# Optimization experiments

Hardware: AMD Instinct MI355X
Metric: run time of the kernel (lower is better)

Reference implementation:

```python
import jax, jax.numpy as jnp
import numpy as np

D_MODEL = 2048
NUM_HEADS = 16
D_KV = D_MODEL // NUM_HEADS
THETA = 10000.0


def apply_rope(x, pos):
    # x: [B, H, S, d_kv], pos: [S] int
    d = x.shape[-1]
    inv_freq = 1.0 / (THETA ** (jnp.arange(0, d, 2, dtype=jnp.float32) / d))  # [d/2]
    ang = pos.astype(jnp.float32)[:, None] * inv_freq[None, :]  # [S, d/2]
    cos, sin = jnp.cos(ang), jnp.sin(ang)  # broadcast over B,H
    x1 = x[..., 0::2]
    x2 = x[..., 1::2]
    r1 = x1 * cos - x2 * sin
    r2 = x1 * sin + x2 * cos
    return jnp.stack([r1, r2], axis=-1).reshape(x.shape)


def setup_inputs() -> dict:
    key = jax.random.key(0)
    k = jax.random.split(key, 5)
    B, S = 2, 2048
    x = jax.random.normal(k[0], (B, S, D_MODEL), dtype=jnp.float32)
    scale = 1.0 / np.sqrt(D_MODEL)
    Wq = jax.random.normal(k[1], (D_MODEL, D_MODEL), dtype=jnp.float32) * scale
    Wk = jax.random.normal(k[2], (D_MODEL, D_MODEL), dtype=jnp.float32) * scale
    Wv = jax.random.normal(k[3], (D_MODEL, D_MODEL), dtype=jnp.float32) * scale
    Wo = jax.random.normal(k[4], (D_MODEL, D_MODEL), dtype=jnp.float32) * scale
    token_position = jnp.arange(S, dtype=jnp.int64 if jax.config.jax_enable_x64 else jnp.int32)
    return {"x": x, "Wq": Wq, "Wk": Wk, "Wv": Wv, "Wo": Wo, "token_position": token_position}


def reference(x, Wq, Wk, Wv, Wo, token_position):
    B, S, _ = x.shape
    def heads(y):
        return y.reshape(B, S, NUM_HEADS, D_KV).transpose(0, 2, 1, 3)  # [B,H,S,d]
    Q = heads(jnp.einsum('bsd,df->bsf', x, Wq))
    K = heads(jnp.einsum('bsd,df->bsf', x, Wk))
    V = heads(jnp.einsum('bsd,df->bsf', x, Wv))
    Q = apply_rope(Q, token_position)
    K = apply_rope(K, token_position)
    scale = 1.0 / jnp.sqrt(jnp.asarray(D_KV, dtype=x.dtype))
    scores = jnp.einsum('bhqd,bhkd->bhqk', Q, K) * scale  # [B,H,S,S]
    causal = jnp.tril(jnp.ones((S, S), dtype=bool))
    scores = jnp.where(causal, scores, -jnp.inf)
    attn = jax.nn.softmax(scores, axis=-1)
    out = jnp.einsum('bhqk,bhkd->bhqd', attn, V)  # [B,H,S,d]
    out = out.transpose(0, 2, 1, 3).reshape(B, S, D_MODEL)
    return jnp.einsum('bsd,df->bsf', out, Wo)
```

## Files before the change

kernel.cpp:

```cpp
#include <hip/hip_runtime.h>
#include <hip/hip_bf16.h>

#define S 2048
#define DM 2048
#define NH 16
#define DH 128

typedef __attribute__((ext_vector_type(8))) short short8;
typedef __attribute__((ext_vector_type(4))) float floatx4;
typedef unsigned short u16;
typedef unsigned int u32;

__device__ __forceinline__ u16 f2bf(float f) {
  union { float f; u32 u; } v; v.f = f;
  u32 r = v.u + 0x7fffu + ((v.u >> 16) & 1u);
  return (u16)(r >> 16);
}
__device__ __forceinline__ u32 pack2(float lo, float hi) {
  float2 f; f.x = lo; f.y = hi;
  __hip_bfloat162 h = __float22bfloat162_rn(f);
  union { __hip_bfloat162 h; u32 u; } c; c.h = h;
  return c.u;
}

__device__ __forceinline__ floatx4 mfma16(short8 a, short8 b, floatx4 c) {
  return __builtin_amdgcn_mfma_f32_16x16x32_bf16(a, b, c, 0, 0, 0);
}

__device__ __forceinline__ void async_cp16(const u16* g, u16* l) {
  __builtin_amdgcn_global_load_lds(
      (const __attribute__((address_space(1))) void*)g,
      (__attribute__((address_space(3))) void*)l, 16, 0, 0);
}

__global__ void conv_x_k(const float* __restrict__ x, u16* __restrict__ xb) {
  int gid = blockIdx.x * 256 + threadIdx.x;
  float4 v = ((const float4*)x)[gid];
  uint2 p; p.x = pack2(v.x, v.y); p.y = pack2(v.z, v.w);
  ((uint2*)xb)[gid] = p;
}

__global__ void conv_w_k(const float* __restrict__ W0, const float* __restrict__ W1,
                         const float* __restrict__ W2, const float* __restrict__ W3,
                         u16* __restrict__ out) {
  __shared__ float tile[32][33];
  const float* W = blockIdx.z == 0 ? W0 : blockIdx.z == 1 ? W1 : blockIdx.z == 2 ? W2 : W3;
  u16* O = out + (size_t)blockIdx.z * DM * DM;
  int tx = threadIdx.x & 31, ty = threadIdx.x >> 5;
  int k0 = blockIdx.y * 32, n0 = blockIdx.x * 32;
#pragma unroll
  for (int j = 0; j < 4; j++)
    tile[ty + j * 8][tx] = W[(size_t)(k0 + ty + j * 8) * DM + n0 + tx];
  __syncthreads();
#pragma unroll
  for (int j = 0; j < 4; j++)
    O[(size_t)(n0 + ty + j * 8) * DM + k0 + tx] = f2bf(tile[tx][ty + j * 8]);
}

#define BM 256
#define BN 256
#define BK 64

#define BARRIER __builtin_amdgcn_s_barrier()
#define SB __builtin_amdgcn_sched_barrier(0)
#define LGKM0 asm volatile("s_waitcnt lgkmcnt(0)" ::: "memory")

#define STG_A(q, j, koff) \
  async_cp16(pAg + (size_t)(j) * 64 * DM + (koff), &As[q][soff + (j) * 4096])
#define STG_B(q, j, koff) \
  async_cp16(pBg + (size_t)(j) * 64 * DM + (koff), &Bs[q][soff + (j) * 4096])

#define PH0(p, q, koff, PRE) { \
    a0k0 = *(const short8*)&As[p][awb + xk0]; \
    a0k1 = *(const short8*)&As[p][awb + xk1]; \
    a1k0 = *(const short8*)&As[p][awb + 1024 + xk0]; \
    a1k1 = *(const short8*)&As[p][awb + 1024 + xk1]; \
    a2k0 = *(const short8*)&As[p][awb + 2048 + xk0]; \
    a2k1 = *(const short8*)&As[p][awb + 2048 + xk1]; \
    a3k0 = *(const short8*)&As[p][awb + 3072 + xk0]; \
    a3k1 = *(const short8*)&As[p][awb + 3072 + xk1]; \
    b0k0 = *(const short8*)&Bs[p][bwb + xk0]; \
    b0k1 = *(const short8*)&Bs[p][bwb + xk1]; \
    b1k0 = *(const short8*)&Bs[p][bwb + 1024 + xk0]; \
    b1k1 = *(const short8*)&Bs[p][bwb + 1024 + xk1]; \
    if (PRE) { STG_A(q, 0, koff); STG_A(q, 1, koff); \
               STG_A(q, 2, koff); STG_A(q, 3, koff); } \
    BARRIER; LGKM0; SB; \
    __builtin_amdgcn_s_setprio(1); \
    acc[0][0] = mfma16(a0k0, b0k0, acc[0][0]); \
    acc[1][0] = mfma16(a1k0, b0k0, acc[1][0]); \
    acc[2][0] = mfma16(a2k0, b0k0, acc[2][0]); \
    acc[3][0] = mfma16(a3k0, b0k0, acc[3][0]); \
    acc[0][1] = mfma16(a0k0, b1k0, acc[0][1]); \
    acc[1][1] = mfma16(a1k0, b1k0, acc[1][1]); \
    acc[2][1] = mfma16(a2k0, b1k0, acc[2][1]); \
    acc[3][1] = mfma16(a3k0, b1k0, acc[3][1]); \
    acc[0][0] = mfma16(a0k1, b0k1, acc[0][0]); \
    acc[1][0] = mfma16(a1k1, b0k1, acc[1][0]); \
    acc[2][0] = mfma16(a2k1, b0k1, acc[2][0]); \
    acc[3][0] = mfma16(a3k1, b0k1, acc[3][0]); \
    acc[0][1] = mfma16(a0k1, b1k1, acc[0][1]); \
    acc[1][1] = mfma16(a1k1, b1k1, acc[1][1]); \
    acc[2][1] = mfma16(a2k1, b1k1, acc[2][1]); \
    acc[3][1] = mfma16(a3k1, b1k1, acc[3][1]); \
    __builtin_amdgcn_s_setprio(0); \
    BARRIER; }

#define PH1(p, q, koff, PRE) { \
    b2k0 = *(const short8*)&Bs[p][bwb + 2048 + xk0]; \
    b2k1 = *(const short8*)&Bs[p][bwb + 2048 + xk1]; \
    b3k0 = *(const short8*)&Bs[p][bwb + 3072 + xk0]; \
    b3k1 = *(const short8*)&Bs[p][bwb + 3072 + xk1]; \
    if (PRE) { STG_B(q, 0, koff); STG_B(q, 1, koff); \
               STG_B(q, 2, koff); STG_B(q, 3, koff); } \
    BARRIER; LGKM0; SB; \
    __builtin_amdgcn_s_setprio(1); \
    acc[0][2] = mfma16(a0k0, b2k0, acc[0][2]); \
    acc[1][2] = mfma16(a1k0, b2k0, acc[1][2]); \
    acc[2][2] = mfma16(a2k0, b2k0, acc[2][2]); \
    acc[3][2] = mfma16(a3k0, b2k0, acc[3][2]); \
    acc[0][3] = mfma16(a0k0, b3k0, acc[0][3]); \
    acc[1][3] = mfma16(a1k0, b3k0, acc[1][3]); \
    acc[2][3] = mfma16(a2k0, b3k0, acc[2][3]); \
    acc[3][3] = mfma16(a3k0, b3k0, acc[3][3]); \
    acc[0][2] = mfma16(a0k1, b2k1, acc[0][2]); \
    acc[1][2] = mfma16(a1k1, b2k1, acc[1][2]); \
    acc[2][2] = mfma16(a2k1, b2k1, acc[2][2]); \
    acc[3][2] = mfma16(a3k1, b2k1, acc[3][2]); \
    acc[0][3] = mfma16(a0k1, b3k1, acc[0][3]); \
    acc[1][3] = mfma16(a1k1, b3k1, acc[1][3]); \
    acc[2][3] = mfma16(a2k1, b3k1, acc[2][3]); \
    acc[3][3] = mfma16(a3k1, b3k1, acc[3][3]); \
    __builtin_amdgcn_s_setprio(0); \
    BARRIER; }

#define PH2(p) { \
    a0k0 = *(const short8*)&As[p][awb + 4096 + xk0]; \
    a0k1 = *(const short8*)&As[p][awb + 4096 + xk1]; \
    a1k0 = *(const short8*)&As[p][awb + 5120 + xk0]; \
    a1k1 = *(const short8*)&As[p][awb + 5120 + xk1]; \
    a2k0 = *(const short8*)&As[p][awb + 6144 + xk0]; \
    a2k1 = *(const short8*)&As[p][awb + 6144 + xk1]; \
    a3k0 = *(const short8*)&As[p][awb + 7168 + xk0]; \
    a3k1 = *(const short8*)&As[p][awb + 7168 + xk1]; \
    BARRIER; LGKM0; SB; \
    __builtin_amdgcn_s_setprio(1); \
    acc[4][0] = mfma16(a0k0, b0k0, acc[4][0]); \
    acc[5][0] = mfma16(a1k0, b0k0, acc[5][0]); \
    acc[6][0] = mfma16(a2k0, b0k0, acc[6][0]); \
    acc[7][0] = mfma16(a3k0, b0k0, acc[7][0]); \
    acc[4][1] = mfma16(a0k0, b1k0, acc[4][1]); \
    acc[5][1] = mfma16(a1k0, b1k0, acc[5][1]); \
    acc[6][1] = mfma16(a2k0, b1k0, acc[6][1]); \
    acc[7][1] = mfma16(a3k0, b1k0, acc[7][1]); \
    acc[4][0] = mfma16(a0k1, b0k1, acc[4][0]); \
    acc[5][0] = mfma16(a1k1, b0k1, acc[5][0]); \
    acc[6][0] = mfma16(a2k1, b0k1, acc[6][0]); \
    acc[7][0] = mfma16(a3k1, b0k1, acc[7][0]); \
    acc[4][1] = mfma16(a0k1, b1k1, acc[4][1]); \
    acc[5][1] = mfma16(a1k1, b1k1, acc[5][1]); \
    acc[6][1] = mfma16(a2k1, b1k1, acc[6][1]); \
    acc[7][1] = mfma16(a3k1, b1k1, acc[7][1]); \
    __builtin_amdgcn_s_setprio(0); \
    BARRIER; }

#define PH3(PRE) { \
    __builtin_amdgcn_s_setprio(1); \
    acc[4][2] = mfma16(a0k0, b2k0, acc[4][2]); \
    acc[5][2] = mfma16(a1k0, b2k0, acc[5][2]); \
    acc[6][2] = mfma16(a2k0, b2k0, acc[6][2]); \
    acc[7][2] = mfma16(a3k0, b2k0, acc[7][2]); \
    acc[4][3] = mfma16(a0k0, b3k0, acc[4][3]); \
    acc[5][3] = mfma16(a1k0, b3k0, acc[5][3]); \
    acc[6][3] = mfma16(a2k0, b3k0, acc[6][3]); \
    acc[7][3] = mfma16(a3k0, b3k0, acc[7][3]); \
    acc[4][2] = mfma16(a0k1, b2k1, acc[4][2]); \
    acc[5][2] = mfma16(a1k1, b2k1, acc[5][2]); \
    acc[6][2] = mfma16(a2k1, b2k1, acc[6][2]); \
    acc[7][2] = mfma16(a3k1, b2k1, acc[7][2]); \
    acc[4][3] = mfma16(a0k1, b3k1, acc[4][3]); \
    acc[5][3] = mfma16(a1k1, b3k1, acc[5][3]); \
    acc[6][3] = mfma16(a2k1, b3k1, acc[6][3]); \
    acc[7][3] = mfma16(a3k1, b3k1, acc[7][3]); \
    __builtin_amdgcn_s_setprio(0); SB; \
    if (PRE) { asm volatile("s_waitcnt vmcnt(0)" ::: "memory"); BARRIER; SB; } }

#define TILE(p, q, koff, PRE) \
    PH0(p, q, koff, PRE) PH1(p, q, koff, PRE) PH2(p) PH3(PRE)

__global__ __launch_bounds__(512, 2)
void gemm_k(const u16* __restrict__ A, const u16* __restrict__ Wt,
            u16* __restrict__ oQ, u16* __restrict__ oK, u16* __restrict__ oV,
            const int* __restrict__ tp)
{
  __shared__ u16 As[2][BM * BK];
  __shared__ u16 Bs[2][BN * BK];
  const int t = threadIdx.x;
  const int w = t >> 6, lane = t & 63;
  const int l16 = lane & 15, quad = lane >> 4;
  const int wr = w >> 2, wc = w & 3;
  const int m0 = blockIdx.y * BM, n0 = blockIdx.x * BN;
  const u16* Bt = Wt + (size_t)blockIdx.z * DM * DM;

  const int srow = t >> 3;
  const int sc = ((t & 7) ^ (srow & 7)) * 8;
  const u16* pAg = A + (size_t)(m0 + srow) * DM + sc;
  const u16* pBg = Bt + (size_t)(n0 + srow) * DM + sc;
  const int soff = t * 8;

  const int awb = (wr * 128 + l16) * 64;
  const int bwb = (wc * 64 + l16) * 64;
  const int xk0 = ((quad) ^ (l16 & 7)) << 3;
  const int xk1 = ((4 + quad) ^ (l16 & 7)) << 3;

  floatx4 acc[8][4] = {};
  short8 a0k0, a0k1, a1k0, a1k1, a2k0, a2k1, a3k0, a3k1;
  short8 b0k0, b0k1, b1k0, b1k1, b2k0, b2k1, b3k0, b3k1;

#pragma unroll
  for (int j = 0; j < 4; j++) STG_A(0, j, 0);
#pragma unroll
  for (int j = 0; j < 4; j++) STG_B(0, j, 0);
  SB;
  asm volatile("s_waitcnt vmcnt(0)" ::: "memory");
  BARRIER; SB;

  for (int it = 0; it < 16; ++it) {
    const int kA = (2 * it + 1) * 64;
    const int kB = (2 * it + 2) * 64;
    TILE(0, 1, kA, 1)
    TILE(1, 0, kB, it < 15)
  }

  const int mwb = m0 + wr * 128;
  const int nwb = n0 + wc * 64;
  if ((int)blockIdx.z == 2) {
#pragma unroll
    for (int mi = 0; mi < 8; mi++) {
      int m = mwb + mi * 16 + quad * 4;
      int b = m >> 11, s = m & (S - 1);
#pragma unroll
      for (int ni = 0; ni < 4; ni++) {
        int f = nwb + ni * 16 + l16;
        int h = f >> 7, dh = f & (DH - 1);
        uint2 pk; pk.x = pack2(acc[mi][ni][0], acc[mi][ni][1]);
        pk.y = pack2(acc[mi][ni][2], acc[mi][ni][3]);
        *(uint2*)&oV[((size_t)(b * NH + h) * DH + dh) * S + s] = pk;
      }
    }
  } else {
    u16* Out = ((int)blockIdx.z == 0) ? oQ : oK;
    const float qs = ((int)blockIdx.z == 0) ? 0.12752780f : 1.0f;
#pragma unroll
    for (int mi = 0; mi < 8; mi++) {
#pragma unroll
      for (int r = 0; r < 4; r++) {
        int m = mwb + mi * 16 + quad * 4 + r;
        int b = m >> 11, s = m & (S - 1);
        int ps = tp[s];
#pragma unroll
        for (int ni = 0; ni < 4; ni++) {
          int f = nwb + ni * 16 + l16;
          int h = f >> 7, dh = f & (DH - 1);
          float own = acc[mi][ni][r];
          float oth = __shfl_xor(own, 1, 64);
          float fr = __expf((float)(dh & ~1) * (-9.210340371976184f / 128.0f));
          float ang = (float)ps * fr;
          float sn, cs; __sincosf(ang, &sn, &cs);
          float res = (dh & 1) ? (oth * sn + own * cs) : (own * cs - oth * sn);
          Out[((size_t)(b * NH + h) * S + s) * DH + dh] = f2bf(res * qs);
        }
      }
    }
  }
}

__global__ __launch_bounds__(256, 4)
void oproj_k(const u16* __restrict__ A, const u16* __restrict__ Wt,
             float* __restrict__ oO)
{
  __shared__ u16 As2[128 * 32];
  __shared__ u16 Bs2[128 * 32];
  const int t = threadIdx.x;
  const int w = t >> 6, lane = t & 63;
  const int l16 = lane & 15, quad = lane >> 4;
  const int m0 = blockIdx.y * 128, n0 = blockIdx.x * 128;
  const int wm = (w >> 1) * 64, wn = (w & 1) * 64;
  const u16* Bt = Wt + (size_t)3 * DM * DM;

  const u16* pA[2]; const u16* pB[2]; u16* lA[2]; u16* lB[2];
#pragma unroll
  for (int i = 0; i < 2; i++) {
    int unit = i * 256 + t;
    int row = unit >> 2, s = unit & 3;
    int c = s ^ ((row >> 1) & 3);
    pA[i] = A + (size_t)(m0 + row) * DM + c * 8;
    pB[i] = Bt + (size_t)(n0 + row) * DM + c * 8;
    lA[i] = &As2[unit * 8];
    lB[i] = &Bs2[unit * 8];
  }

  floatx4 acc[4][4] = {};

  for (int k0 = 0; k0 < DM; k0 += 32) {
#pragma unroll
    for (int i = 0; i < 2; i++) {
      async_cp16(pA[i] + k0, lA[i]);
      async_cp16(pB[i] + k0, lB[i]);
    }
    __syncthreads();
    short8 af[4], bfr[4];
#pragma unroll
    for (int i = 0; i < 4; i++) {
      int row = wm + i * 16 + l16;
      af[i] = *(short8*)&As2[(row * 4 + (quad ^ ((row >> 1) & 3))) * 8];
    }
#pragma unroll
    for (int i = 0; i < 4; i++) {
      int row = wn + i * 16 + l16;
      bfr[i] = *(short8*)&Bs2[(row * 4 + (quad ^ ((row >> 1) & 3))) * 8];
    }
#pragma unroll
    for (int mi = 0; mi < 4; mi++)
#pragma unroll
      for (int ni = 0; ni < 4; ni++)
        acc[mi][ni] = mfma16(af[mi], bfr[ni], acc[mi][ni]);
    __syncthreads();
  }

#pragma unroll
  for (int mi = 0; mi < 4; mi++) {
    int m = m0 + wm + mi * 16 + quad * 4;
#pragma unroll
    for (int ni = 0; ni < 4; ni++) {
      int n = n0 + wn + ni * 16 + l16;
#pragma unroll
      for (int r = 0; r < 4; r++)
        oO[(size_t)(m + r) * DM + n] = acc[mi][ni][r];
    }
  }
}

__global__ __launch_bounds__(256, 4)
void attn_k(const u16* __restrict__ Q, const u16* __restrict__ K,
            const u16* __restrict__ Vt, u16* __restrict__ O)
{
  __shared__ u16 Ks[64 * 128];
  __shared__ u16 Vs[128 * 64];
  __shared__ u16 P[4][16 * 64];
  const int t = threadIdx.x, w = t >> 6, lane = t & 63;
  const int l16 = lane & 15, quad = lane >> 4;
  const int task = blockIdx.x;
  const int bh = task & 31, b = bh >> 4, h = bh & 15;
  const int g = 31 - (task >> 5);
  const int qg = g * 64;
  const int qt = qg + w * 16;
  const u16* Qb = Q + (size_t)bh * S * DH;
  const u16* Kb = K + (size_t)bh * S * DH;
  const u16* Vb = Vt + (size_t)bh * DH * S;
  u16* Pw = P[w];
  const int pxor = l16 & 7;

  const u16* pK[4]; u16* lK[4];
  const u16* pV[4]; u16* lV[4];
#pragma unroll
  for (int j = 0; j < 4; j++) {
    int kr = w * 16 + j * 4 + (lane >> 4);
    int ks = lane & 15;
    int kc = ks ^ (kr & 15);
    pK[j] = Kb + (size_t)kr * DH + kc * 8;
    lK[j] = &Ks[kr * 128 + ks * 8];
    int vr = w * 32 + j * 8 + (lane >> 3);
    int vs = lane & 7;
    int vc = vs ^ (vr & 7);
    pV[j] = Vb + (size_t)vr * S + vc * 8;
    lV[j] = &Vs[vr * 64 + vs * 8];
  }

  short8 aq[4];
#pragma unroll
  for (int kc = 0; kc < 4; kc++)
    aq[kc] = *(const short8*)&Qb[(size_t)(qt + l16) * DH + kc * 32 + quad * 8];

  floatx4 o[8] = {};
  float lsum = 0.0f;
  const int kend = qg + 64;

  for (int k0 = 0; k0 < kend; k0 += 64) {
#pragma unroll
    for (int j = 0; j < 4; j++) async_cp16(pK[j] + (size_t)k0 * DH, lK[j]);
#pragma unroll
    for (int j = 0; j < 4; j++) async_cp16(pV[j] + k0, lV[j]);
    __syncthreads();

    floatx4 sc[4] = {};
    __builtin_amdgcn_s_setprio(1);
#pragma unroll
    for (int hh = 0; hh < 4; hh++) {
      int row = hh * 16 + l16;
#pragma unroll
      for (int kc = 0; kc < 4; kc++) {
        short8 kf = *(short8*)&Ks[row * 128 + (((kc * 4 + quad) ^ l16) << 3)];
        sc[hh] = mfma16(kf, aq[kc], sc[hh]);
      }
    }
    __builtin_amdgcn_s_setprio(0);
    if (k0 + 64 > qt) {
#pragma unroll
      for (int hh = 0; hh < 4; hh++)
#pragma unroll
        for (int r = 0; r < 4; r++) {
          int j = k0 + hh * 16 + quad * 4 + r;
          if (j > qt + l16) sc[hh][r] = -3.0e38f;
        }
    }
#pragma unroll
    for (int hh = 0; hh < 4; hh++) {
      float e0 = __builtin_amdgcn_exp2f(fminf(sc[hh][0], 44.0f));
      float e1 = __builtin_amdgcn_exp2f(fminf(sc[hh][1], 44.0f));
      float e2 = __builtin_amdgcn_exp2f(fminf(sc[hh][2], 44.0f));
      float e3 = __builtin_amdgcn_exp2f(fminf(sc[hh][3], 44.0f));
      lsum += (e0 + e1) + (e2 + e3);
      uint2 pk; pk.x = pack2(e0, e1); pk.y = pack2(e2, e3);
      int su = (2 * hh + (quad >> 1)) ^ pxor;
      *(uint2*)&Pw[l16 * 64 + su * 8 + (quad & 1) * 4] = pk;
    }
    asm volatile("s_waitcnt lgkmcnt(0)" ::: "memory");
    __builtin_amdgcn_s_setprio(1);
#pragma unroll
    for (int c = 0; c < 2; c++) {
      short8 pf = *(short8*)&Pw[l16 * 64 + (((4 * c + quad) ^ pxor) << 3)];
#pragma unroll
      for (int t8 = 0; t8 < 8; t8++) {
        int row = t8 * 16 + l16;
        short8 av = *(short8*)&Vs[row * 64 + (((c * 4 + quad) ^ (l16 & 7)) << 3)];
        o[t8] = mfma16(av, pf, o[t8]);
      }
    }
    __builtin_amdgcn_s_setprio(0);
    __syncthreads();
  }

  float l = lsum + __shfl_xor(lsum, 16, 64);
  l += __shfl_xor(l, 32, 64);
  float inv = __builtin_amdgcn_rcpf(l);
#pragma unroll
  for (int t8 = 0; t8 < 8; t8++) {
    uint2 pa;
    pa.x = pack2(o[t8][0] * inv, o[t8][1] * inv);
    pa.y = pack2(o[t8][2] * inv, o[t8][3] * inv);
    *(uint2*)&O[((size_t)(b * S + qt + l16)) * DM + h * DH + t8 * 16 + quad * 4] = pa;
  }
}

extern "C" void kernel_launch(void* const* d_in, const int* in_sizes, int n_in,
                              void* d_out, int out_size, void* d_ws, size_t ws_size,
                              hipStream_t stream) {
  const float* x  = (const float*)d_in[0];
  const float* Wq = (const float*)d_in[1];
  const float* Wk = (const float*)d_in[2];
  const float* Wv = (const float*)d_in[3];
  const float* Wo = (const float*)d_in[4];
  const int*   tp = (const int*)d_in[5];

  char* ws = (char*)d_ws;
  u16* Wt = (u16*)ws;
  u16* xb = (u16*)(ws + 33554432);
  u16* Qb = (u16*)(ws + 50331648);
  u16* Kb = (u16*)(ws + 67108864);
  u16* Vb = (u16*)(ws + 83886080);
  u16* Ob = (u16*)(ws + 100663296);

  conv_x_k<<<8192, 256, 0, stream>>>(x, xb);
  conv_w_k<<<dim3(64, 64, 4), 256, 0, stream>>>(Wq, Wk, Wv, Wo, Wt);
  gemm_k<<<dim3(8, 16, 3), 512, 0, stream>>>(xb, Wt, Qb, Kb, Vb, tp);
  attn_k<<<1024, 256, 0, stream>>>(Qb, Kb, Vb, Ob);
  oproj_k<<<dim3(16, 32), 256, 0, stream>>>(Ob, Wt, (float*)d_out);
}
```

Baseline: 378.3 us.

## Deepen GEMM prefetch: load tile k+2 into same buffer after reads finish

Restructures the double-buffered QKV projection GEMM so both buffers are filled up front, and each tile's next-next K slice is loaded into the buffer just consumed. B loads are issued in phase 2, after the B fragments are read, and A loads in phase 3, after the A fragments are read. The wait changes from vmcnt(0) to vmcnt(8), so one tile of loads stays in flight across the barrier. This is meant to hide more global-load latency behind the MFMAs. In exchange it depends on every load for a buffer being issued only after all waves have finished reading that buffer, and on the vmcnt counting being exact.

Result: faster. 370.1 us (-2.2%).

```diff
diff --git a/kernel.cpp b/kernel.cpp
--- a/kernel.cpp
+++ b/kernel.cpp
@@ -70,7 +70,7 @@
 #define STG_B(q, j, koff) \
   async_cp16(pBg + (size_t)(j) * 64 * DM + (koff), &Bs[q][soff + (j) * 4096])
 
-#define PH0(p, q, koff, PRE) { \
+#define PH0(p) { \
     a0k0 = *(const short8*)&As[p][awb + xk0]; \
     a0k1 = *(const short8*)&As[p][awb + xk1]; \
     a1k0 = *(const short8*)&As[p][awb + 1024 + xk0]; \
@@ -83,8 +83,6 @@
     b0k1 = *(const short8*)&Bs[p][bwb + xk1]; \
     b1k0 = *(const short8*)&Bs[p][bwb + 1024 + xk0]; \
     b1k1 = *(const short8*)&Bs[p][bwb + 1024 + xk1]; \
-    if (PRE) { STG_A(q, 0, koff); STG_A(q, 1, koff); \
-               STG_A(q, 2, koff); STG_A(q, 3, koff); } \
     BARRIER; LGKM0; SB; \
     __builtin_amdgcn_s_setprio(1); \
     acc[0][0] = mfma16(a0k0, b0k0, acc[0][0]); \
@@ -106,13 +104,11 @@
     __builtin_amdgcn_s_setprio(0); \
     BARRIER; }
 
-#define PH1(p, q, koff, PRE) { \
+#define PH1(p) { \
     b2k0 = *(const short8*)&Bs[p][bwb + 2048 + xk0]; \
     b2k1 = *(const short8*)&Bs[p][bwb + 2048 + xk1]; \
     b3k0 = *(const short8*)&Bs[p][bwb + 3072 + xk0]; \
     b3k1 = *(const short8*)&Bs[p][bwb + 3072 + xk1]; \
-    if (PRE) { STG_B(q, 0, koff); STG_B(q, 1, koff); \
-               STG_B(q, 2, koff); STG_B(q, 3, koff); } \
     BARRIER; LGKM0; SB; \
     __builtin_amdgcn_s_setprio(1); \
     acc[0][2] = mfma16(a0k0, b2k0, acc[0][2]); \
@@ -134,7 +130,7 @@
     __builtin_amdgcn_s_setprio(0); \
     BARRIER; }
 
-#define PH2(p) { \
+#define PH2(p, koff2, PRE2) { \
     a0k0 = *(const short8*)&As[p][awb + 4096 + xk0]; \
     a0k1 = *(const short8*)&As[p][awb + 4096 + xk1]; \
     a1k0 = *(const short8*)&As[p][awb + 5120 + xk0]; \
@@ -143,6 +139,8 @@
     a2k1 = *(const short8*)&As[p][awb + 6144 + xk1]; \
     a3k0 = *(const short8*)&As[p][awb + 7168 + xk0]; \
     a3k1 = *(const short8*)&As[p][awb + 7168 + xk1]; \
+    if (PRE2) { STG_B(p, 0, koff2); STG_B(p, 1, koff2); \
+                STG_B(p, 2, koff2); STG_B(p, 3, koff2); } \
     BARRIER; LGKM0; SB; \
     __builtin_amdgcn_s_setprio(1); \
     acc[4][0] = mfma16(a0k0, b0k0, acc[4][0]); \
@@ -164,7 +162,10 @@
     __builtin_amdgcn_s_setprio(0); \
     BARRIER; }
 
-#define PH3(PRE) { \
+#define PH3(p, koff2, PRE2, LAST) { \
+    if (PRE2) { STG_A(p, 0, koff2); STG_A(p, 1, koff2); \
+                STG_A(p, 2, koff2); STG_A(p, 3, koff2); } \
+    SB; \
     __builtin_amdgcn_s_setprio(1); \
     acc[4][2] = mfma16(a0k0, b2k0, acc[4][2]); \
     acc[5][2] = mfma16(a1k0, b2k0, acc[5][2]); \
@@ -183,10 +184,13 @@
     acc[6][3] = mfma16(a2k1, b3k1, acc[6][3]); \
     acc[7][3] = mfma16(a3k1, b3k1, acc[7][3]); \
     __builtin_amdgcn_s_setprio(0); SB; \
-    if (PRE) { asm volatile("s_waitcnt vmcnt(0)" ::: "memory"); BARRIER; SB; } }
-
-#define TILE(p, q, koff, PRE) \
-    PH0(p, q, koff, PRE) PH1(p, q, koff, PRE) PH2(p) PH3(PRE)
+    if (!LAST) { \
+      if (PRE2) { asm volatile("s_waitcnt vmcnt(8)" ::: "memory"); } \
+      else      { asm volatile("s_waitcnt vmcnt(0)" ::: "memory"); } \
+      BARRIER; SB; } }
+
+#define TILE(p, koff2, PRE2, LAST) \
+    PH0(p) PH1(p) PH2(p, koff2, PRE2) PH3(p, koff2, PRE2, LAST)
 
 __global__ __launch_bounds__(512, 2)
 void gemm_k(const u16* __restrict__ A, const u16* __restrict__ Wt,
@@ -221,16 +225,22 @@
   for (int j = 0; j < 4; j++) STG_A(0, j, 0);
 #pragma unroll
   for (int j = 0; j < 4; j++) STG_B(0, j, 0);
+#pragma unroll
+  for (int j = 0; j < 4; j++) STG_A(1, j, BK);
+#pragma unroll
+  for (int j = 0; j < 4; j++) STG_B(1, j, BK);
   SB;
-  asm volatile("s_waitcnt vmcnt(0)" ::: "memory");
+  asm volatile("s_waitcnt vmcnt(8)" ::: "memory");
   BARRIER; SB;
 
-  for (int it = 0; it < 16; ++it) {
-    const int kA = (2 * it + 1) * 64;
-    const int kB = (2 * it + 2) * 64;
-    TILE(0, 1, kA, 1)
-    TILE(1, 0, kB, it < 15)
-  }
+  for (int it = 0; it < 15; ++it) {
+    const int kE = (2 * it + 2) * 64;
+    const int kO = (2 * it + 3) * 64;
+    TILE(0, kE, 1, 0)
+    TILE(1, kO, 1, 0)
+  }
+  TILE(0, 0, 0, 0)
+  TILE(1, 0, 0, 1)
 
   const int mwb = m0 + wr * 128;
   const int nwb = n0 + wc * 64;
```
